# Kernel tuning notes

Measured on AMD Instinct MI355X. Metric: run time of the kernel, lower is better.

## Reference

```python
import jax, jax.numpy as jnp
import numpy as np
from jax.scipy.linalg import expm

D = 12   # Fock cutoff dimension
M = 4    # qumodes per circuit
L = 2    # CVNN layers
K = M * (M - 1) // 2  # beamsplitters per interferometer
B = 1024

def _lad():
    # annihilation operator a in truncated Fock basis
    return jnp.diag(jnp.sqrt(jnp.arange(1, D, dtype=jnp.float32)), k=1).astype(jnp.complex64)

def _disp_gen(rr, ph):
    # generator of Displacement(r, phi): alpha*adag - conj(alpha)*a
    lad = _lad()
    alpha = (rr * jnp.exp(1j * ph)).astype(jnp.complex64)
    return alpha * lad.conj().T - jnp.conj(alpha) * lad

def _squeeze_mat(rr, ph):
    lad = _lad()
    z = (rr * jnp.exp(1j * ph)).astype(jnp.complex64)
    a2 = lad @ lad
    return expm(0.5 * (jnp.conj(z) * a2 - z * a2.conj().T))

def _rot_diag(ph):
    n = jnp.arange(D, dtype=jnp.float32)
    return jnp.exp(1j * ph * n).astype(jnp.complex64)

def _kerr_diag(kap):
    n = jnp.arange(D, dtype=jnp.float32)
    return jnp.exp(1j * kap * n * n).astype(jnp.complex64)

def _bs_mat(th, ph):
    # Beamsplitter exp(theta*(e^{i phi} a b^dag - e^{-i phi} a^dag b)) on D^2 space
    lad = _lad()
    eye = jnp.eye(D, dtype=jnp.complex64)
    a1 = jnp.kron(lad, eye)
    a2 = jnp.kron(eye, lad)
    H = th * (jnp.exp(1j * ph) * (a1 @ a2.conj().T) - jnp.exp(-1j * ph) * (a1.conj().T @ a2))
    return expm(H.astype(jnp.complex64)).reshape(D, D, D, D)

def _apply_1mode(psi, U, mode):
    psi = jnp.moveaxis(psi, mode + 1, -1)
    psi = psi @ U.T
    return jnp.moveaxis(psi, -1, mode + 1)

def _apply_1mode_batched(psi, U, mode):
    psi = jnp.moveaxis(psi, mode + 1, -1)
    psi = jnp.einsum('bij,b...j->b...i', U, psi)
    return jnp.moveaxis(psi, -1, mode + 1)

def _apply_diag(psi, d, mode):
    shape = [1] * psi.ndim
    shape[mode + 1] = D
    return psi * d.reshape(shape)

def _apply_2mode(psi, G, mode):
    psi = jnp.moveaxis(psi, (mode + 1, mode + 2), (-2, -1))
    psi = jnp.einsum('ijkl,...kl->...ij', G, psi)
    return jnp.moveaxis(psi, (-2, -1), (mode + 1, mode + 2))

def _interferometer(psi, theta, phi, varphi):
    # PennyLane rectangular (Clements) mesh, then per-mode rotations
    n = 0
    for ll in range(M):
        for kk in range(M - 1):
            if (ll + kk) % 2 != 1:
                psi = _apply_2mode(psi, _bs_mat(theta[n], phi[n]), kk)
                n += 1
    for m in range(M):
        psi = _apply_diag(psi, _rot_diag(varphi[m]), m)
    return psi

def _forward(x, theta_1, phi_1, varphi_1, r, phi_r, theta_2, phi_2, varphi_2, a, phi_a, k):
    b = x.shape[0]
    psi = jnp.zeros((b,) + (D,) * M, dtype=jnp.complex64)
    psi = psi.at[(slice(None),) + (0,) * M].set(1.0)  # vacuum
    # Amplitude_Phase encoding: Displacement(x[:, m], x[:, m+M]) on mode m
    for m in range(M):
        U = jax.vmap(lambda rr, ph: expm(_disp_gen(rr, ph)))(x[:, m], x[:, m + M])
        psi = _apply_1mode_batched(psi, U, m)
    # CVNeuralNetLayers
    for l in range(L):
        psi = _interferometer(psi, theta_1[l], phi_1[l], varphi_1[l])
        for m in range(M):
            psi = _apply_1mode(psi, _squeeze_mat(r[l, m], phi_r[l, m]), m)
        psi = _interferometer(psi, theta_2[l], phi_2[l], varphi_2[l])
        for m in range(M):
            psi = _apply_1mode(psi, expm(_disp_gen(a[l, m], phi_a[l, m])), m)
            psi = _apply_diag(psi, _kerr_diag(k[l, m]), m)
    # X-quadrature expvals (SF convention hbar=2: X = a + adag)
    lad = _lad()
    Xmat = lad + lad.conj().T
    sum_axes = tuple(range(1, M + 1))
    outs = [jnp.real(jnp.sum(jnp.conj(psi) * _apply_1mode(psi, Xmat, m), axis=sum_axes)) for m in range(M)]
    return jnp.stack(outs, axis=1)

def setup_inputs():
    key = jax.random.key(0)
    ks = jax.random.split(key, 12)
    tp = 2.0 * np.pi
    return {
        'x': jax.random.normal(ks[0], (B, 2 * M), dtype=jnp.float32),
        'theta_1': tp * jax.random.uniform(ks[1], (L, K), dtype=jnp.float32),
        'phi_1': tp * jax.random.uniform(ks[2], (L, K), dtype=jnp.float32),
        'varphi_1': tp * jax.random.uniform(ks[3], (L, M), dtype=jnp.float32),
        'r': 0.1 * jax.random.uniform(ks[4], (L, M), dtype=jnp.float32),
        'phi_r': tp * jax.random.uniform(ks[5], (L, M), dtype=jnp.float32),
        'theta_2': tp * jax.random.uniform(ks[6], (L, K), dtype=jnp.float32),
        'phi_2': tp * jax.random.uniform(ks[7], (L, K), dtype=jnp.float32),
        'varphi_2': tp * jax.random.uniform(ks[8], (L, M), dtype=jnp.float32),
        'a': 0.1 * jax.random.uniform(ks[9], (L, M), dtype=jnp.float32),
        'phi_a': tp * jax.random.uniform(ks[10], (L, M), dtype=jnp.float32),
        'k': tp * jax.random.uniform(ks[11], (L, M), dtype=jnp.float32),
    }

def reference(x, theta_1, phi_1, varphi_1, r, phi_r, theta_2, phi_2, varphi_2, a, phi_a, k):
    return _forward(x, theta_1, phi_1, varphi_1, r, phi_r, theta_2, phi_2, varphi_2, a, phi_a, k)
```

## Files before the change

kernel.cpp:

```cpp
#include <hip/hip_runtime.h>
#include <math.h>

#define D4 20736
#define ST 14
#define SST 168
#define KP 18

typedef float c32 __attribute__((ext_vector_type(2)));

__device__ __forceinline__ c32 C2(float x, float y) { c32 r; r.x = x; r.y = y; return r; }
#define CZERO C2(0.f, 0.f)

__device__ __forceinline__ c32 cmul(c32 a, c32 b) {
  return C2(a.x * b.x - a.y * b.y, a.x * b.y + a.y * b.x);
}
__device__ __forceinline__ c32 cfma_s(c32 a, c32 b, c32 acc) {
  acc.x = fmaf(a.x, b.x, fmaf(-a.y, b.y, acc.x));
  acc.y = fmaf(a.x, b.y, fmaf(a.y, b.x, acc.y));
  return acc;
}
__device__ __forceinline__ c32 cfma(c32 g, c32 v, c32 acc) {
  c32 t, d;
  asm("v_pk_fma_f32 %0, %1, %2, %3 op_sel_hi:[0,1,1]"
      : "=v"(t) : "v"(g), "v"(v), "v"(acc));
  asm("v_pk_fma_f32 %0, %1, %2, %3 op_sel:[1,1,0] op_sel_hi:[1,0,1] neg_lo:[1,0,0]"
      : "=v"(d) : "v"(g), "v"(v), "v"(t));
  return d;
}
__device__ __forceinline__ c32 get2(const float4* w, int n) {
  float4 q = w[n >> 1];
  return (n & 1) ? C2(q.z, q.w) : C2(q.x, q.y);
}
__device__ __forceinline__ float4 pack2(c32 a, c32 b) {
  return make_float4(a.x, a.y, b.x, b.y);
}

__constant__ int d_secoff[24] = {0,1,5,14,30,55,91,140,204,285,385,506,650,
                                 771,871,952,1016,1065,1101,1126,1142,1151,1155,1156};

__constant__ unsigned char d_pp[78] = {
  88,89,90,91,92,93,
  80,81,82,83,84,85,
  96,97,98,99,100,101,
  72,73,74,75,76,
  104,105,106,107,108,
  64,65,66,67,68,
  112,113,114,115,116,
  56,57,58,59,
  120,121,122,123,
  48,49,50,51,
  128,129,130,131,
  40,41,42,
  136,137,138,
  32,33,34,
  144,145,146,
  24,25,
  152,153,
  16,17,
  160,161,
  8,
  168,
  0,
  176
};

struct PM { int sz, goff, a0, da, r0, dr, w1, w2; bool v1; };
__device__ __forceinline__ PM pmeta(int pr) {
  const int code = d_pp[pr];
  const int N = code >> 3, k = code & 7;
  const bool up = (N <= 11);
  PM m;
  m.sz = (up ? N : 22 - N) + 1;
  const int lo = up ? 0 : (N - 11);
  const int i0 = lo + 2 * k;
  m.v1 = (2 * k + 1 < m.sz);
  m.goff = d_secoff[N] + 2 * k;
  m.a0 = up ? N : (143 + N);
  m.da = up ? 13 : -13;
  m.r0 = up ? N : (121 + N);
  m.dr = up ? 11 : -11;
  m.w1 = 13 * i0 + N;
  m.w2 = 11 * i0 + N;
  return m;
}

__device__ void small_expm(c32* A, c32* S, c32* P, c32* T, float* red, int sz, int tid) {
  const int n2 = sz * sz;
  if (tid < sz) {
    float s = 0.f;
    for (int j = 0; j < sz; ++j) { c32 v = A[tid * sz + j]; s += sqrtf(fmaf(v.x, v.x, v.y * v.y)); }
    red[tid] = s;
  }
  __syncthreads();
  float nrm = 0.f;
  for (int i = 0; i < sz; ++i) nrm = fmaxf(nrm, red[i]);
  int sp = 0;
  while (nrm > 0.35f && sp < 24) { nrm *= 0.5f; ++sp; }
  const float scale = ldexpf(1.f, -sp);
  for (int e = tid; e < n2; e += 64) { A[e].x *= scale; A[e].y *= scale; }
  __syncthreads();
  for (int e = tid; e < n2; e += 64) {
    c32 a = A[e];
    P[e] = a;
    if ((e / sz) == (e % sz)) a.x += 1.f;
    S[e] = a;
  }
  __syncthreads();
  for (int k = 2; k <= 12; ++k) {
    const float inv = 1.f / (float)k;
    for (int e = tid; e < n2; e += 64) {
      int i = e / sz, j = e - i * sz;
      c32 acc = CZERO;
      for (int q = 0; q < sz; ++q) acc = cfma_s(P[i * sz + q], A[q * sz + j], acc);
      acc.x *= inv; acc.y *= inv;
      T[e] = acc;
    }
    __syncthreads();
    for (int e = tid; e < n2; e += 64) {
      c32 t = T[e];
      P[e] = t;
      S[e].x += t.x; S[e].y += t.y;
    }
    __syncthreads();
  }
  for (int q = 0; q < sp; ++q) {
    for (int e = tid; e < n2; e += 64) {
      int i = e / sz, j = e - i * sz;
      c32 acc = CZERO;
      for (int w = 0; w < sz; ++w) acc = cfma_s(S[i * sz + w], S[w * sz + j], acc);
      T[e] = acc;
    }
    __syncthreads();
    for (int e = tid; e < n2; e += 64) S[e] = T[e];
    __syncthreads();
  }
}

__global__ __launch_bounds__(64) void prep_disp(const float* __restrict__ x, c32* __restrict__ c0) {
  __shared__ c32 A[144], S[144], P[144], T[144];
  __shared__ float red[12];
  const int tid = threadIdx.x;
  const int b = blockIdx.x >> 2, m = blockIdx.x & 3;
  const float rr = x[b * 8 + m], ph = x[b * 8 + 4 + m];
  float sn, cs;
  sincosf(ph, &sn, &cs);
  const c32 alpha = C2(rr * cs, rr * sn);
  for (int e = tid; e < 144; e += 64) A[e] = CZERO;
  __syncthreads();
  if (tid < 11) {
    float sq = sqrtf((float)(tid + 1));
    A[(tid + 1) * 12 + tid] = C2(alpha.x * sq, alpha.y * sq);
    A[tid * 12 + tid + 1] = C2(-alpha.x * sq, alpha.y * sq);
  }
  __syncthreads();
  small_expm(A, S, P, T, red, 12, tid);
  if (tid < 12) c0[(size_t)blockIdx.x * 12 + tid] = S[tid * 12];
}

__global__ __launch_bounds__(64) void prep_bs(const float* __restrict__ th1, const float* __restrict__ ph1,
                                              const float* __restrict__ th2, const float* __restrict__ ph2,
                                              c32* __restrict__ BS) {
  __shared__ c32 A[144], S[144], P[144], T[144];
  __shared__ float red[12];
  const int tid = threadIdx.x;
  const int g = blockIdx.x / 23, N = blockIdx.x % 23;
  const int l = g / 12, rem = g % 12, w = rem / 6, gi = rem % 6;
  const float th = (w ? th2 : th1)[l * 6 + gi];
  const float ph = (w ? ph2 : ph1)[l * 6 + gi];
  const int lo = (N > 11) ? (N - 11) : 0;
  const int sz = (N <= 11) ? (N + 1) : (23 - N);
  float sn, cs;
  sincosf(ph, &sn, &cs);
  for (int e = tid; e < sz * sz; e += 64) A[e] = CZERO;
  __syncthreads();
  if (tid + 1 < sz) {
    int t = tid + 1;
    float s1 = th * sqrtf((float)((lo + t) * (N - lo - t + 1)));
    A[(t - 1) * sz + t] = C2(cs * s1, sn * s1);
    A[t * sz + t - 1] = C2(-cs * s1, sn * s1);
  }
  __syncthreads();
  small_expm(A, S, P, T, red, sz, tid);
  c32* dst = BS + (size_t)g * 1156 + d_secoff[N];
  const bool upSec = (N <= 11);
  for (int e = tid; e < sz * sz; e += 64) {
    int p = e / sz, q = e - p * sz;
    int qs = upSec ? q : (sz - 1 - q);
    dst[q * sz + p] = S[p * sz + qs];
  }
}

__global__ __launch_bounds__(64) void prep_p(const float* __restrict__ r_, const float* __restrict__ phir,
                                             const float* __restrict__ vphi1,
                                             const float* __restrict__ a_, const float* __restrict__ phia,
                                             const float* __restrict__ vphi2, const float* __restrict__ kk,
                                             c32* __restrict__ P1, c32* __restrict__ P2) {
  __shared__ c32 A[144], S[144], P[144], T[144];
  __shared__ float red[12];
  const int tid = threadIdx.x;
  const int which = blockIdx.x >> 3, lm = blockIdx.x & 7;
  for (int e = tid; e < 144; e += 64) A[e] = CZERO;
  __syncthreads();
  if (which == 0) {
    const float rv = r_[lm], pv = phir[lm];
    float sn, cs;
    sincosf(pv, &sn, &cs);
    const c32 z = C2(rv * cs, rv * sn);
    if (tid < 10) {
      float sq = 0.5f * sqrtf((float)((tid + 1) * (tid + 2)));
      A[tid * 12 + tid + 2] = C2(z.x * sq, -z.y * sq);
      A[(tid + 2) * 12 + tid] = C2(-z.x * sq, -z.y * sq);
    }
  } else {
    const float av = a_[lm], pv = phia[lm];
    float sn, cs;
    sincosf(pv, &sn, &cs);
    const c32 alpha = C2(av * cs, av * sn);
    if (tid < 11) {
      float sq = sqrtf((float)(tid + 1));
      A[(tid + 1) * 12 + tid] = C2(alpha.x * sq, alpha.y * sq);
      A[tid * 12 + tid + 1] = C2(-alpha.x * sq, alpha.y * sq);
    }
  }
  __syncthreads();
  small_expm(A, S, P, T, red, 12, tid);
  if (which == 0) {
    const float vp = vphi1[lm];
    for (int e = tid; e < 144; e += 64) {
      int j = e % 12;
      float sn, cs;
      sincosf(vp * (float)j, &sn, &cs);
      P1[(size_t)lm * 144 + e] = cmul(S[e], C2(cs, sn));
    }
  } else {
    const float vp = vphi2[lm], kv = kk[lm];
    for (int e = tid; e < 144; e += 64) {
      int i = e / 12, j = e % 12;
      float sn1, cs1, sn2, cs2;
      sincosf(vp * (float)j, &sn1, &cs1);
      float ang = kv * (float)i;
      ang *= (float)i;
      sincosf(ang, &sn2, &cs2);
      P2[(size_t)lm * 144 + e] = cmul(C2(cs2, sn2), cmul(S[e], C2(cs1, sn1)));
    }
  }
}

__global__ __launch_bounds__(256, 6) void k123_kernel(
    c32* __restrict__ psi,
    const c32* __restrict__ gbs23, const c32* __restrict__ gbs12,
    const c32* __restrict__ gu1, const c32* __restrict__ gu2, const c32* __restrict__ gu3) {
  __shared__ __align__(16) c32 buf[2016];
  __shared__ c32 gate[1168];
  const int tid = threadIdx.x;
  c32 pf[5];
#pragma unroll
  for (int k = 0; k < 5; ++k) {
    int e = tid + 256 * k;
    pf[k] = (e < 1156) ? gbs12[e] : CZERO;
  }
  c32 pf3 = (gu3 && tid < 144) ? gu3[tid] : CZERO;
  if (gu1) for (int e = tid; e < 144; e += 256) buf[ST * ((e % 12) * 12 + e / 12) + 12] = gu1[e];
  if (gu2) for (int e = tid; e < 144; e += 256) buf[ST * ((e % 12) * 12 + e / 12) + 13] = gu2[e];
  for (int e = tid; e < 1156; e += 256) gate[e] = gbs23[e];
  c32* slab = psi + (size_t)blockIdx.x * 1728;
  for (int v = tid; v < 864; v += 256) {
    float4 q = ((const float4*)slab)[v];
    *((float4*)buf + 7 * (v / 6) + (v % 6)) = q;
  }
  __syncthreads();
  const int pr = tid >> 1, h = tid & 1;
  PM m;
  if (tid < 156) m = pmeta(pr);
  c32 acc0[6], acc1[6];
  if (tid < 156) {
#pragma unroll
    for (int n = 0; n < 6; ++n) { acc0[n] = CZERO; acc1[n] = CZERO; }
    int a = m.a0 + 1008 * h, go = m.goff;
    for (int t = 0; t < m.sz; ++t) {
      c32 g0 = gate[go];
      c32 g1 = gate[go + 1];
      if (!m.v1) g1 = CZERO;
      go += m.sz;
#pragma unroll
      for (int n = 0; n < 6; ++n) {
        c32 v = buf[SST * n + a];
        acc0[n] = cfma(g0, v, acc0[n]);
        acc1[n] = cfma(g1, v, acc1[n]);
      }
      a += m.da;
    }
  }
  __syncthreads();
  if (tid < 156) {
    const int w0 = m.w1 + 1008 * h;
#pragma unroll
    for (int n = 0; n < 6; ++n) buf[SST * n + w0] = acc0[n];
    if (m.v1) {
#pragma unroll
      for (int n = 0; n < 6; ++n) buf[SST * n + w0 + 13] = acc1[n];
    }
  }
#pragma unroll
  for (int k = 0; k < 5; ++k) {
    int e = tid + 256 * k;
    if (e < 1156) gate[e] = pf[k];
  }
  __syncthreads();
  if (tid < 156) {
#pragma unroll
    for (int n = 0; n < 6; ++n) { acc0[n] = CZERO; acc1[n] = CZERO; }
    int rho = m.r0, go = m.goff;
    for (int t = 0; t < m.sz; ++t) {
      c32 g0 = gate[go];
      c32 g1 = gate[go + 1];
      if (!m.v1) g1 = CZERO;
      go += m.sz;
      const float4* ip = (const float4*)buf + 7 * rho + 3 * h;
      float4 w0 = ip[0], w1 = ip[1], w2 = ip[2];
      c32 v[6] = {C2(w0.x,w0.y), C2(w0.z,w0.w), C2(w1.x,w1.y),
                  C2(w1.z,w1.w), C2(w2.x,w2.y), C2(w2.z,w2.w)};
#pragma unroll
      for (int n = 0; n < 6; ++n) {
        acc0[n] = cfma(g0, v[n], acc0[n]);
        acc1[n] = cfma(g1, v[n], acc1[n]);
      }
      rho += m.dr;
    }
  }
  __syncthreads();
  if (tid < 156) {
    float4* opA = (float4*)buf + 7 * m.w2 + 3 * h;
    opA[0] = pack2(acc0[0], acc0[1]);
    opA[1] = pack2(acc0[2], acc0[3]);
    opA[2] = pack2(acc0[4], acc0[5]);
    if (m.v1) {
      float4* opB = (float4*)buf + 7 * (m.w2 + 11) + 3 * h;
      opB[0] = pack2(acc1[0], acc1[1]);
      opB[1] = pack2(acc1[2], acc1[3]);
      opB[2] = pack2(acc1[4], acc1[5]);
    }
  }
  if (gu3 && tid < 144) gate[tid] = pf3;
  if (gu1) {
    __syncthreads();
    if (tid < 144) {
      const int p = tid >> 1, hh = tid & 1;
      const int k2 = p / 12, n2 = p - 12 * (p / 12);
#pragma unroll
      for (int n = 0; n < 6; ++n) { acc0[n] = CZERO; acc1[n] = CZERO; }
#pragma unroll
      for (int j = 0; j < 12; ++j) {
        c32 g0 = buf[ST * (j * 12 + 2 * k2) + 12];
        c32 g1 = buf[ST * (j * 12 + 2 * k2 + 1) + 12];
        const float4* ip = (const float4*)buf + 7 * (12 * j + n2) + 3 * hh;
        float4 w0 = ip[0], w1 = ip[1], w2 = ip[2];
        c32 v[6] = {C2(w0.x,w0.y), C2(w0.z,w0.w), C2(w1.x,w1.y),
                    C2(w1.z,w1.w), C2(w2.x,w2.y), C2(w2.z,w2.w)};
#pragma unroll
        for (int n = 0; n < 6; ++n) {
          acc0[n] = cfma(g0, v[n], acc0[n]);
          acc1[n] = cfma(g1, v[n], acc1[n]);
        }
      }
    }
    __syncthreads();
    if (tid < 144) {
      const int p = tid >> 1, hh = tid & 1;
      const int k2 = p / 12, n2 = p - 12 * (p / 12);
      float4* opA = (float4*)buf + 7 * ((2 * k2) * 12 + n2) + 3 * hh;
      float4* opB = (float4*)buf + 7 * ((2 * k2 + 1) * 12 + n2) + 3 * hh;
      opA[0] = pack2(acc0[0], acc0[1]); opA[1] = pack2(acc0[2], acc0[3]); opA[2] = pack2(acc0[4], acc0[5]);
      opB[0] = pack2(acc1[0], acc1[1]); opB[1] = pack2(acc1[2], acc1[3]); opB[2] = pack2(acc1[4], acc1[5]);
    }
  }
  if (gu2) {
    __syncthreads();
    if (tid < 144) {
      const int p = tid >> 1, hh = tid & 1;
      const int n1 = p / 6, k2 = p - 6 * (p / 6);
#pragma unroll
      for (int n = 0; n < 6; ++n) { acc0[n] = CZERO; acc1[n] = CZERO; }
#pragma unroll
      for (int j = 0; j < 12; ++j) {
        c32 g0 = buf[ST * (j * 12 + 2 * k2) + 13];
        c32 g1 = buf[ST * (j * 12 + 2 * k2 + 1) + 13];
        const float4* ip = (const float4*)buf + 7 * (12 * n1 + j) + 3 * hh;
        float4 w0 = ip[0], w1 = ip[1], w2 = ip[2];
        c32 v[6] = {C2(w0.x,w0.y), C2(w0.z,w0.w), C2(w1.x,w1.y),
                    C2(w1.z,w1.w), C2(w2.x,w2.y), C2(w2.z,w2.w)};
#pragma unroll
        for (int n = 0; n < 6; ++n) {
          acc0[n] = cfma(g0, v[n], acc0[n]);
          acc1[n] = cfma(g1, v[n], acc1[n]);
        }
      }
    }
    __syncthreads();
    if (tid < 144) {
      const int p = tid >> 1, hh = tid & 1;
      const int n1 = p / 6, k2 = p - 6 * (p / 6);
      float4* opA = (float4*)buf + 7 * (12 * n1 + 2 * k2) + 3 * hh;
      float4* opB = (float4*)buf + 7 * (12 * n1 + 2 * k2 + 1) + 3 * hh;
      opA[0] = pack2(acc0[0], acc0[1]); opA[1] = pack2(acc0[2], acc0[3]); opA[2] = pack2(acc0[4], acc0[5]);
      opB[0] = pack2(acc1[0], acc1[1]); opB[1] = pack2(acc1[2], acc1[3]); opB[2] = pack2(acc1[4], acc1[5]);
    }
  }
  if (gu3) {
    __syncthreads();
    if (tid < 144) {
      const float4* ip = (const float4*)buf + 7 * tid;
      float4 wv[6];
#pragma unroll
      for (int q = 0; q < 6; ++q) wv[q] = ip[q];
      float4* op = (float4*)buf + 7 * tid;
#pragma unroll
      for (int cpair = 0; cpair < 6; ++cpair) {
        c32 s0 = CZERO, s1 = CZERO;
#pragma unroll
        for (int j = 0; j < 12; ++j) {
          c32 v = get2(wv, j);
          s0 = cfma(gate[(2 * cpair) * 12 + j], v, s0);
          s1 = cfma(gate[(2 * cpair + 1) * 12 + j], v, s1);
        }
        op[cpair] = pack2(s0, s1);
      }
    }
  }
  __syncthreads();
  for (int v = tid; v < 864; v += 256) {
    ((float4*)slab)[v] = *((const float4*)buf + 7 * (v / 6) + (v % 6));
  }
}

__global__ __launch_bounds__(256, 5) void k01_kernel(
    c32* __restrict__ psi, const c32* __restrict__ c0,
    const c32* __restrict__ gu0, const c32* __restrict__ gbs) {
  __shared__ __align__(16) c32 buf[2592];
  __shared__ c32 gate[1168];
  __shared__ c32 cv[4][12];
  const int tid = threadIdx.x;
  const int b = blockIdx.x / 9, t = blockIdx.x % 9;
  if (gu0) for (int e = tid; e < 144; e += 256) buf[KP * ((e % 12) * 12 + e / 12) + 16] = gu0[e];
  if (gbs) for (int e = tid; e < 1156; e += 256) gate[e] = gbs[e];
  c32* gbase = psi + (size_t)b * D4 + t * 16;
  if (c0) {
    if (tid < 48) cv[tid / 12][tid % 12] = c0[(size_t)b * 48 + tid];
    __syncthreads();
    for (int e = tid; e < 2304; e += 256) {
      int row = e >> 4, q = e & 15;
      int cc = 16 * t + q, n2 = cc / 12, n3 = cc - 12 * n2;
      buf[KP * row + q] =
          cmul(cmul(cv[0][row / 12], cv[1][row % 12]), cmul(cv[2][n2], cv[3][n3]));
    }
  } else {
    for (int e = tid; e < 1152; e += 256) {
      int row = e >> 3, q = e & 7;
      ((float4*)(buf + row * KP))[q] = ((const float4*)(gbase + (size_t)row * 144))[q];
    }
  }
  __syncthreads();
  c32 acc0[8], acc1[8];
  if (gu0) {
    if (tid < 144) {
      const int p = tid >> 1, hh = tid & 1;
      const int k2 = p / 12, n1 = p - 12 * (p / 12);
#pragma unroll
      for (int n = 0; n < 8; ++n) { acc0[n] = CZERO; acc1[n] = CZERO; }
#pragma unroll
      for (int j = 0; j < 12; ++j) {
        c32 g0 = buf[KP * (j * 12 + 2 * k2) + 16];
        c32 g1 = buf[KP * (j * 12 + 2 * k2 + 1) + 16];
        const float4* ip = (const float4*)(buf + (12 * j + n1) * KP) + 4 * hh;
        float4 w[4];
#pragma unroll
        for (int q = 0; q < 4; ++q) w[q] = ip[q];
#pragma unroll
        for (int n = 0; n < 8; ++n) {
          c32 v = get2(w, n);
          acc0[n] = cfma(g0, v, acc0[n]);
          acc1[n] = cfma(g1, v, acc1[n]);
        }
      }
    }
    __syncthreads();
    if (tid < 144) {
      const int p = tid >> 1, hh = tid & 1;
      const int k2 = p / 12, n1 = p - 12 * (p / 12);
      float4* opA = (float4*)(buf + ((2 * k2) * 12 + n1) * KP) + 4 * hh;
      float4* opB = (float4*)(buf + ((2 * k2 + 1) * 12 + n1) * KP) + 4 * hh;
#pragma unroll
      for (int q = 0; q < 4; ++q) {
        opA[q] = pack2(acc0[2 * q], acc0[2 * q + 1]);
        opB[q] = pack2(acc1[2 * q], acc1[2 * q + 1]);
      }
    }
    __syncthreads();
  }
  if (gbs) {
    const int pr = tid >> 1, h = tid & 1;
    PM m;
    if (tid < 156) {
      m = pmeta(pr);
#pragma unroll
      for (int n = 0; n < 8; ++n) { acc0[n] = CZERO; acc1[n] = CZERO; }
      int rho = m.r0, go = m.goff;
      for (int tk = 0; tk < m.sz; ++tk) {
        c32 g0 = gate[go];
        c32 g1 = gate[go + 1];
        if (!m.v1) g1 = CZERO;
        go += m.sz;
        const float4* ip = (const float4*)(buf + rho * KP) + 4 * h;
        float4 w[4];
#pragma unroll
        for (int q = 0; q < 4; ++q) w[q] = ip[q];
#pragma unroll
        for (int n = 0; n < 8; ++n) {
          c32 v = get2(w, n);
          acc0[n] = cfma(g0, v, acc0[n]);
          acc1[n] = cfma(g1, v, acc1[n]);
        }
        rho += m.dr;
      }
    }
    __syncthreads();
    if (tid < 156) {
      float4* opA = (float4*)(buf + m.w2 * KP) + 4 * h;
#pragma unroll
      for (int q = 0; q < 4; ++q) opA[q] = pack2(acc0[2 * q], acc0[2 * q + 1]);
      if (m.v1) {
        float4* opB = (float4*)(buf + (m.w2 + 11) * KP) + 4 * h;
#pragma unroll
        for (int q = 0; q < 4; ++q) opB[q] = pack2(acc1[2 * q], acc1[2 * q + 1]);
      }
    }
    __syncthreads();
  }
  for (int e = tid; e < 1152; e += 256) {
    int row = e >> 3, q = e & 7;
    ((float4*)(gbase + (size_t)row * 144))[q] = ((const float4*)(buf + row * KP))[q];
  }
}

__global__ __launch_bounds__(256) void expval_kernel(const c32* __restrict__ psi, float* __restrict__ out) {
  __shared__ float red[1024];
  __shared__ float sq2[12];
  const int tid = threadIdx.x, b = blockIdx.x;
  if (tid < 12) sq2[tid] = 2.f * sqrtf((float)(tid + 1));
  __syncthreads();
  const c32* base = psi + (size_t)b * D4;
  float a0 = 0.f, a1 = 0.f, a2 = 0.f, a3 = 0.f;
  for (int e = tid; e < D4; e += 256) {
    c32 p = base[e];
    int n3 = e % 12, t = e / 12;
    int n2 = t % 12; t /= 12;
    int n1 = t % 12, n0 = t / 12;
    if (n3 < 11) { c32 q = base[e + 1];    a3 = fmaf(sq2[n3], fmaf(p.x, q.x, p.y * q.y), a3); }
    if (n2 < 11) { c32 q = base[e + 12];   a2 = fmaf(sq2[n2], fmaf(p.x, q.x, p.y * q.y), a2); }
    if (n1 < 11) { c32 q = base[e + 144];  a1 = fmaf(sq2[n1], fmaf(p.x, q.x, p.y * q.y), a1); }
    if (n0 < 11) { c32 q = base[e + 1728]; a0 = fmaf(sq2[n0], fmaf(p.x, q.x, p.y * q.y), a0); }
  }
  red[tid * 4 + 0] = a0; red[tid * 4 + 1] = a1; red[tid * 4 + 2] = a2; red[tid * 4 + 3] = a3;
  __syncthreads();
  for (int s = 128; s > 0; s >>= 1) {
    if (tid < s) {
      red[tid * 4 + 0] += red[(tid + s) * 4 + 0];
      red[tid * 4 + 1] += red[(tid + s) * 4 + 1];
      red[tid * 4 + 2] += red[(tid + s) * 4 + 2];
      red[tid * 4 + 3] += red[(tid + s) * 4 + 3];
    }
    __syncthreads();
  }
  if (tid < 4) out[b * 4 + tid] = red[tid];
}

extern "C" void kernel_launch(void* const* d_in, const int* in_sizes, int n_in,
                              void* d_out, int out_size, void* d_ws, size_t ws_size,
                              hipStream_t stream) {
  const float* x      = (const float*)d_in[0];
  const float* theta1 = (const float*)d_in[1];
  const float* phi1   = (const float*)d_in[2];
  const float* vphi1  = (const float*)d_in[3];
  const float* r_     = (const float*)d_in[4];
  const float* phir   = (const float*)d_in[5];
  const float* theta2 = (const float*)d_in[6];
  const float* phi2   = (const float*)d_in[7];
  const float* vphi2  = (const float*)d_in[8];
  const float* a_     = (const float*)d_in[9];
  const float* phia   = (const float*)d_in[10];
  const float* kk     = (const float*)d_in[11];
  float* out = (float*)d_out;

  const size_t PSI_OFF = 0;
  const size_t C0_OFF  = 169869312;
  const size_t P1_OFF  = C0_OFF + 393216;
  const size_t P2_OFF  = P1_OFF + 9216;
  const size_t BS_OFF  = P2_OFF + 9216;
  const size_t NEED    = BS_OFF + 221952;
  if (ws_size < NEED) return;

  char* ws = (char*)d_ws;
  c32* psi = (c32*)(ws + PSI_OFF);
  c32* c0  = (c32*)(ws + C0_OFF);
  c32* P1  = (c32*)(ws + P1_OFF);
  c32* P2  = (c32*)(ws + P2_OFF);
  c32* BS  = (c32*)(ws + BS_OFF);

  prep_disp<<<dim3(4096), dim3(64), 0, stream>>>(x, c0);
  prep_bs<<<dim3(552), dim3(64), 0, stream>>>(theta1, phi1, theta2, phi2, BS);
  prep_p<<<dim3(16), dim3(64), 0, stream>>>(r_, phir, vphi1, a_, phia, vphi2, kk, P1, P2);

  for (int l = 0; l < 2; ++l) {
    c32* bsl = BS + (size_t)l * 12 * 1156;
    const c32* c0arg = (l == 0) ? c0 : (const c32*)nullptr;
    const c32* u0pre = (l == 0) ? (const c32*)nullptr : (const c32*)(P2 + (size_t)(l - 1) * 4 * 144);
    k01_kernel<<<dim3(9216), dim3(256), 0, stream>>>(psi, c0arg, u0pre, bsl + 0 * 1156);
    k123_kernel<<<dim3(12288), dim3(256), 0, stream>>>(psi, bsl + 1 * 1156, bsl + 2 * 1156,
                                                       nullptr, nullptr, nullptr);
    k01_kernel<<<dim3(9216), dim3(256), 0, stream>>>(psi, nullptr, nullptr, bsl + 3 * 1156);
    k123_kernel<<<dim3(12288), dim3(256), 0, stream>>>(psi, bsl + 4 * 1156, bsl + 5 * 1156,
                                                       P1 + (size_t)(l * 4 + 1) * 144,
                                                       P1 + (size_t)(l * 4 + 2) * 144,
                                                       P1 + (size_t)(l * 4 + 3) * 144);
    k01_kernel<<<dim3(9216), dim3(256), 0, stream>>>(psi, nullptr, P1 + (size_t)(l * 4 + 0) * 144, bsl + 6 * 1156);
    k123_kernel<<<dim3(12288), dim3(256), 0, stream>>>(psi, bsl + 7 * 1156, bsl + 8 * 1156,
                                                       nullptr, nullptr, nullptr);
    k01_kernel<<<dim3(9216), dim3(256), 0, stream>>>(psi, nullptr, nullptr, bsl + 9 * 1156);
    k123_kernel<<<dim3(12288), dim3(256), 0, stream>>>(psi, bsl + 10 * 1156, bsl + 11 * 1156,
                                                       P2 + (size_t)(l * 4 + 1) * 144,
                                                       P2 + (size_t)(l * 4 + 2) * 144,
                                                       P2 + (size_t)(l * 4 + 3) * 144);
  }
  k01_kernel<<<dim3(9216), dim3(256), 0, stream>>>(psi, nullptr, P2 + (size_t)(1 * 4 + 0) * 144, nullptr);
  expval_kernel<<<dim3(1024), dim3(256), 0, stream>>>(psi, out);
}
```

Baseline: 1.888 ms.

## Software-prefetch LDS operands in beamsplitter loops and pair gate entries for float4 loads

Each beamsplitter contraction loop now issues the next iteration's gate and state LDS loads before the current complex FMAs run, hiding LDS latency. The single-mode gate matrices are also repacked in shared memory so each pair of gate coefficients sits contiguously. One vectorized float4 load then replaces two scalar loads. The trade-off is more live registers under a 6-waves-per-SIMD launch bound, plus a harmless extra LDS read past the end on the final loop iteration.

```diff
diff --git a/kernel.cpp b/kernel.cpp
--- a/kernel.cpp
+++ b/kernel.cpp
@@ -260,8 +260,14 @@
     pf[k] = (e < 1156) ? gbs12[e] : CZERO;
   }
   c32 pf3 = (gu3 && tid < 144) ? gu3[tid] : CZERO;
-  if (gu1) for (int e = tid; e < 144; e += 256) buf[ST * ((e % 12) * 12 + e / 12) + 12] = gu1[e];
-  if (gu2) for (int e = tid; e < 144; e += 256) buf[ST * ((e % 12) * 12 + e / 12) + 13] = gu2[e];
+  if (gu1) for (int e = tid; e < 144; e += 256) {
+    int i = e / 12, j = e - 12 * i;
+    buf[ST * (12 * j + (i >> 1)) + 12 + (i & 1)] = gu1[e];
+  }
+  if (gu2) for (int e = tid; e < 144; e += 256) {
+    int i = e / 12, j = e - 12 * i;
+    buf[ST * (12 * j + 6 + (i >> 1)) + 12 + (i & 1)] = gu2[e];
+  }
   for (int e = tid; e < 1156; e += 256) gate[e] = gbs23[e];
   c32* slab = psi + (size_t)blockIdx.x * 1728;
   for (int v = tid; v < 864; v += 256) {
@@ -277,18 +283,27 @@
 #pragma unroll
     for (int n = 0; n < 6; ++n) { acc0[n] = CZERO; acc1[n] = CZERO; }
     int a = m.a0 + 1008 * h, go = m.goff;
+    c32 g0 = gate[go];
+    c32 g1 = m.v1 ? gate[go + 1] : CZERO;
+    c32 v[6];
+#pragma unroll
+    for (int n = 0; n < 6; ++n) v[n] = buf[SST * n + a];
     for (int t = 0; t < m.sz; ++t) {
-      c32 g0 = gate[go];
-      c32 g1 = gate[go + 1];
-      if (!m.v1) g1 = CZERO;
-      go += m.sz;
+      const int an = a + m.da, gon = go + m.sz;
+      c32 ng0 = gate[gon];
+      c32 ng1 = m.v1 ? gate[gon + 1] : CZERO;
+      c32 nv[6];
+#pragma unroll
+      for (int n = 0; n < 6; ++n) nv[n] = buf[SST * n + an];
 #pragma unroll
       for (int n = 0; n < 6; ++n) {
-        c32 v = buf[SST * n + a];
-        acc0[n] = cfma(g0, v, acc0[n]);
-        acc1[n] = cfma(g1, v, acc1[n]);
-      }
-      a += m.da;
+        acc0[n] = cfma(g0, v[n], acc0[n]);
+        acc1[n] = cfma(g1, v[n], acc1[n]);
+      }
+      g0 = ng0; g1 = ng1;
+#pragma unroll
+      for (int n = 0; n < 6; ++n) v[n] = nv[n];
+      a = an; go = gon;
     }
   }
   __syncthreads();
@@ -311,13 +326,22 @@
 #pragma unroll
     for (int n = 0; n < 6; ++n) { acc0[n] = CZERO; acc1[n] = CZERO; }
     int rho = m.r0, go = m.goff;
+    c32 g0 = gate[go];
+    c32 g1 = m.v1 ? gate[go + 1] : CZERO;
+    float4 w0, w1, w2;
+    {
+      const float4* ip = (const float4*)buf + 7 * rho + 3 * h;
+      w0 = ip[0]; w1 = ip[1]; w2 = ip[2];
+    }
     for (int t = 0; t < m.sz; ++t) {
-      c32 g0 = gate[go];
-      c32 g1 = gate[go + 1];
-      if (!m.v1) g1 = CZERO;
-      go += m.sz;
-      const float4* ip = (const float4*)buf + 7 * rho + 3 * h;
-      float4 w0 = ip[0], w1 = ip[1], w2 = ip[2];
+      const int rhon = rho + m.dr, gon = go + m.sz;
+      c32 ng0 = gate[gon];
+      c32 ng1 = m.v1 ? gate[gon + 1] : CZERO;
+      float4 nw0, nw1, nw2;
+      {
+        const float4* ip = (const float4*)buf + 7 * rhon + 3 * h;
+        nw0 = ip[0]; nw1 = ip[1]; nw2 = ip[2];
+      }
       c32 v[6] = {C2(w0.x,w0.y), C2(w0.z,w0.w), C2(w1.x,w1.y),
                   C2(w1.z,w1.w), C2(w2.x,w2.y), C2(w2.z,w2.w)};
 #pragma unroll
@@ -325,7 +349,9 @@
         acc0[n] = cfma(g0, v[n], acc0[n]);
         acc1[n] = cfma(g1, v[n], acc1[n]);
       }
-      rho += m.dr;
+      g0 = ng0; g1 = ng1;
+      w0 = nw0; w1 = nw1; w2 = nw2;
+      rho = rhon; go = gon;
     }
   }
   __syncthreads();
@@ -341,7 +367,7 @@
       opB[2] = pack2(acc1[4], acc1[5]);
     }
   }
-  if (gu3 && tid < 144) gate[tid] = pf3;
+  if (gu3 && tid < 144) gate[(tid % 12) * 12 + (tid / 12)] = pf3;
   if (gu1) {
     __syncthreads();
     if (tid < 144) {
@@ -351,8 +377,8 @@
       for (int n = 0; n < 6; ++n) { acc0[n] = CZERO; acc1[n] = CZERO; }
 #pragma unroll
       for (int j = 0; j < 12; ++j) {
-        c32 g0 = buf[ST * (j * 12 + 2 * k2) + 12];
-        c32 g1 = buf[ST * (j * 12 + 2 * k2 + 1) + 12];
+        float4 gq = *((const float4*)buf + 7 * (12 * j + k2) + 6);
+        c32 g0 = C2(gq.x, gq.y), g1 = C2(gq.z, gq.w);
         const float4* ip = (const float4*)buf + 7 * (12 * j + n2) + 3 * hh;
         float4 w0 = ip[0], w1 = ip[1], w2 = ip[2];
         c32 v[6] = {C2(w0.x,w0.y), C2(w0.z,w0.w), C2(w1.x,w1.y),
@@ -383,8 +409,8 @@
       for (int n = 0; n < 6; ++n) { acc0[n] = CZERO; acc1[n] = CZERO; }
 #pragma unroll
       for (int j = 0; j < 12; ++j) {
-        c32 g0 = buf[ST * (j * 12 + 2 * k2) + 13];
-        c32 g1 = buf[ST * (j * 12 + 2 * k2 + 1) + 13];
+        float4 gq = *((const float4*)buf + 7 * (12 * j + 6 + k2) + 6);
+        c32 g0 = C2(gq.x, gq.y), g1 = C2(gq.z, gq.w);
         const float4* ip = (const float4*)buf + 7 * (12 * n1 + j) + 3 * hh;
         float4 w0 = ip[0], w1 = ip[1], w2 = ip[2];
         c32 v[6] = {C2(w0.x,w0.y), C2(w0.z,w0.w), C2(w1.x,w1.y),
@@ -419,9 +445,10 @@
         c32 s0 = CZERO, s1 = CZERO;
 #pragma unroll
         for (int j = 0; j < 12; ++j) {
+          float4 gq = *((const float4*)gate + 6 * j + cpair);
           c32 v = get2(wv, j);
-          s0 = cfma(gate[(2 * cpair) * 12 + j], v, s0);
-          s1 = cfma(gate[(2 * cpair + 1) * 12 + j], v, s1);
+          s0 = cfma(C2(gq.x, gq.y), v, s0);
+          s1 = cfma(C2(gq.z, gq.w), v, s1);
         }
         op[cpair] = pack2(s0, s1);
       }
@@ -441,7 +468,10 @@
   __shared__ c32 cv[4][12];
   const int tid = threadIdx.x;
   const int b = blockIdx.x / 9, t = blockIdx.x % 9;
-  if (gu0) for (int e = tid; e < 144; e += 256) buf[KP * ((e % 12) * 12 + e / 12) + 16] = gu0[e];
+  if (gu0) for (int e = tid; e < 144; e += 256) {
+    int i = e / 12, j = e - 12 * i;
+    buf[KP * (12 * j + (i >> 1)) + 16 + (i & 1)] = gu0[e];
+  }
   if (gbs) for (int e = tid; e < 1156; e += 256) gate[e] = gbs[e];
   c32* gbase = psi + (size_t)b * D4 + t * 16;
   if (c0) {
@@ -469,8 +499,8 @@
       for (int n = 0; n < 8; ++n) { acc0[n] = CZERO; acc1[n] = CZERO; }
 #pragma unroll
       for (int j = 0; j < 12; ++j) {
-        c32 g0 = buf[KP * (j * 12 + 2 * k2) + 16];
-        c32 g1 = buf[KP * (j * 12 + 2 * k2 + 1) + 16];
+        float4 gq = *((const float4*)buf + 9 * (12 * j + k2) + 8);
+        c32 g0 = C2(gq.x, gq.y), g1 = C2(gq.z, gq.w);
         const float4* ip = (const float4*)(buf + (12 * j + n1) * KP) + 4 * hh;
         float4 w[4];
 #pragma unroll
@@ -505,22 +535,34 @@
 #pragma unroll
       for (int n = 0; n < 8; ++n) { acc0[n] = CZERO; acc1[n] = CZERO; }
       int rho = m.r0, go = m.goff;
+      c32 g0 = gate[go];
+      c32 g1 = m.v1 ? gate[go + 1] : CZERO;
+      float4 w[4];
+      {
+        const float4* ip = (const float4*)(buf + rho * KP) + 4 * h;
+#pragma unroll
+        for (int q = 0; q < 4; ++q) w[q] = ip[q];
+      }
       for (int tk = 0; tk < m.sz; ++tk) {
-        c32 g0 = gate[go];
-        c32 g1 = gate[go + 1];
-        if (!m.v1) g1 = CZERO;
-        go += m.sz;
-        const float4* ip = (const float4*)(buf + rho * KP) + 4 * h;
-        float4 w[4];
-#pragma unroll
-        for (int q = 0; q < 4; ++q) w[q] = ip[q];
+        const int rhon = rho + m.dr, gon = go + m.sz;
+        c32 ng0 = gate[gon];
+        c32 ng1 = m.v1 ? gate[gon + 1] : CZERO;
+        float4 nw[4];
+        {
+          const float4* ip = (const float4*)(buf + rhon * KP) + 4 * h;
+#pragma unroll
+          for (int q = 0; q < 4; ++q) nw[q] = ip[q];
+        }
 #pragma unroll
         for (int n = 0; n < 8; ++n) {
           c32 v = get2(w, n);
           acc0[n] = cfma(g0, v, acc0[n]);
           acc1[n] = cfma(g1, v, acc1[n]);
         }
-        rho += m.dr;
+        g0 = ng0; g1 = ng1;
+#pragma unroll
+        for (int q = 0; q < 4; ++q) w[q] = nw[q];
+        rho = rhon; go = gon;
       }
     }
     __syncthreads();
```

New measurement: 1.836 ms. 2.8% less time.
